# Kernel optimization log

Hardware: AMD Instinct MI355X
Metric: run time of the kernel (lower is better)

The kernel has to match this reference:

```python
import jax, jax.numpy as jnp
import numpy as np

B = 2048   # batch of sampled occupation configurations
L = 64     # nphysical (spatial orbitals / MPS sites)
P = 4      # local physical dimension (2 spin orbitals -> 4 occupations)
D = 128    # MPS bond dimension


def setup_inputs() -> dict:
    key = jax.random.key(0)
    k1, k2, k3, k4 = jax.random.split(key, 4)
    onstate = jax.random.randint(k1, (B, L), 0, P)  # occupation per site
    # flat MPS data buffer reshaped to [site, occupation, Dl, Dr];
    # scale by D**-0.5 so the length-L matrix chain stays O(1).
    site_tensors = jax.random.normal(k2, (L, P, D, D), dtype=jnp.float32) * (D ** -0.5)
    left_vec = jax.random.normal(k3, (D,), dtype=jnp.float32)
    right_vec = jax.random.normal(k4, (D,), dtype=jnp.float32)
    return {
        "onstate": onstate,
        "site_tensors": site_tensors,
        "left_vec": left_vec,
        "right_vec": right_vec,
    }


def reference(onstate, site_tensors, right_vec, left_vec=None, **_ignore):
    # keyword-robust shim not needed; real signature below
    raise NotImplementedError


def reference(onstate, site_tensors, left_vec, right_vec):
    """MPS amplitude: amp[b] = l^T (prod_i A[i, s_{b,i}]) r, evaluated as a
    left-to-right chain of gathered batched vector-matrix products."""
    batch = onstate.shape[0]
    s_seq = onstate.T.astype(jnp.int32)                      # [L, B]
    v0 = jnp.broadcast_to(left_vec, (batch, left_vec.shape[0]))  # [B, D]

    def step(v, inp):
        A_i, s_i = inp            # A_i: [P, D, D], s_i: [B]
        M = A_i[s_i]              # data-dependent gather -> [B, D, D]
        v = jnp.einsum('bd,bde->be', v, M)
        return v, None

    vL, _ = jax.lax.scan(step, v0, (site_tensors, s_seq))
    return vL @ right_vec         # [B] amplitudes
```

## Files before the change

### kernel.cpp

```cpp
#include <hip/hip_runtime.h>
#include <hip/hip_fp16.h>

constexpr int L = 64;
constexpr int P = 4;
constexpr int D = 128;
constexpr int B = 2048;
constexpr int EPW = 16;
constexpr int NG = B / EPW;

using v8h = __attribute__((ext_vector_type(8))) _Float16;
using v4h = __attribute__((ext_vector_type(4))) _Float16;
using v4f = __attribute__((ext_vector_type(4))) float;

constexpr size_t UT_OFF  = 0;
constexpr size_t WT_OFF  = 1048576;
constexpr size_t MTF_OFF = 2097152;
constexpr size_t MTB_OFF = 6291456;

constexpr int VLDS0 = 131072;
constexpr int VLDS1 = 131072 + 4096;
constexpr int PLDS  = 131072 + 8192;
constexpr int SMEM_BYTES = PLDS + L * EPW * 4;

#define WAIT_VM8   0xF78
#define WAIT_VM0   0xF70
#define WAIT_LGKM0 0xC07F

__device__ __forceinline__ void gl2lds16(const void* g, void* l) {
  __builtin_amdgcn_global_load_lds(
      (const __attribute__((address_space(1))) void*)g,
      (__attribute__((address_space(3))) void*)l, 16, 0, 0);
}

__global__ void convert_dual(const float* __restrict__ src,
                             _Float16* __restrict__ mtf,
                             _Float16* __restrict__ mtb) {
  const int mat  = blockIdx.x >> 1;
  const int half = blockIdx.x & 1;
  const int site = mat >> 2;
  const int t = threadIdx.x;
  if (site >= 32) {
    const float4* sb = (const float4*)(src + (size_t)mat * 16384);
    _Float16* bb = mtb + (size_t)(mat - 128) * 16384;
#pragma unroll
    for (int it = 0; it < 8; ++it) {
      int idx = t + (half * 8 + it) * 256;
      float4 f = sb[idx];
      v4h h4 = {(_Float16)f.x, (_Float16)f.y, (_Float16)f.z, (_Float16)f.w};
      *(v4h*)(bb + idx * 4) = h4;
    }
    return;
  }
  const float* sb = src + (size_t)mat * 16384;
  _Float16* fb = mtf + (size_t)mat * 16384;
  const int cl = t & 63;
  const int dg = t >> 6;
  const int c = half * 64 + cl;
#pragma unroll
  for (int dh = 0; dh < 4; ++dh) {
    const int d8 = dh * 4 + dg;
    v8h v;
#pragma unroll
    for (int j = 0; j < 8; ++j) v[j] = (_Float16)sb[(d8 * 8 + j) * D + c];
    *(v8h*)(fb + c * D + d8 * 8) = v;
  }
}

__global__ __launch_bounds__(512, 1) void mps_half_chain(
    const int* __restrict__ onstate, const _Float16* __restrict__ mtf,
    const _Float16* __restrict__ mtb, const float* __restrict__ left_vec,
    const float* __restrict__ right_vec, float* __restrict__ ut,
    float* __restrict__ wt) {
  extern __shared__ char smem[];
  const int tid = threadIdx.x;
  const int wave = tid >> 6, lane = tid & 63;
  const int me = lane & 15, q4 = lane >> 4;
  const bool fwd = !(blockIdx.x & 1);
  const int b0 = (blockIdx.x >> 1) * EPW;
  const _Float16* mbase = fwd ? mtf : mtb;
  const float* ivec = fwd ? left_vec : right_vec;
  float* ovec = fwd ? ut : wt;

  int* plds = (int*)(smem + PLDS);
#pragma unroll
  for (int j = 0; j < 2; ++j) {
    int idx = tid + j * 512;
    int e = idx >> 6, i = idx & 63;
    plds[i * EPW + e] = onstate[(b0 + e) * L + i];
  }
  if (tid < 256) {
    int e = tid >> 4, seg = tid & 15;
    _Float16* vp = (_Float16*)(smem + VLDS0) + e * 128 + (seg ^ (e & 7)) * 8;
#pragma unroll
    for (int j = 0; j < 8; ++j) vp[j] = (_Float16)ivec[seg * 8 + j];
  }

  char* wbuf = smem + wave * 16384;

  int soff[8];
#pragma unroll
  for (int i = 0; i < 8; ++i) {
    int u = i * 64 + lane;
    int p = u >> 7, r = u & 127, cl = r >> 3, slot = r & 7;
    soff[i] = p * 32768 + (wave * 16 + cl) * 256 + (slot ^ (cl & 7)) * 16;
  }
  auto stage = [&](int ls, int h, int z) {
    const char* gb = (const char*)mbase + (size_t)ls * 131072 + h * 128;
    char* lb = wbuf + z * 8192;
#pragma unroll
    for (int i = 0; i < 8; ++i) gl2lds16(gb + soff[i], lb + i * 1024);
  };
  auto consume = [&](int h, int z, int pm, const char* vb, v4f& acc) {
    const int s0 = h * 8 + q4, s1 = h * 8 + 4 + q4;
    v8h a0 = *(const v8h*)(vb + me * 256 + (s0 ^ (me & 7)) * 16);
    v8h a1 = *(const v8h*)(vb + me * 256 + (s1 ^ (me & 7)) * 16);
    const char* cb = wbuf + z * 8192;
#pragma unroll
    for (int p = 0; p < P; ++p) {
      const bool isp = (pm == p);
      v8h zf = {};
      v8h am0 = isp ? a0 : zf;
      v8h am1 = isp ? a1 : zf;
      const char* pb = cb + p * 2048 + me * 128;
      v8h bf0 = *(const v8h*)(pb + ((q4) ^ (me & 7)) * 16);
      v8h bf1 = *(const v8h*)(pb + ((4 + q4) ^ (me & 7)) * 16);
      acc = __builtin_amdgcn_mfma_f32_16x16x32_f16(am0, bf0, acc, 0, 0, 0);
      acc = __builtin_amdgcn_mfma_f32_16x16x32_f16(am1, bf1, acc, 0, 0, 0);
    }
  };

  __syncthreads();
  stage(fwd ? 0 : 31, 0, 0);

  const int c0 = wave * 16 + me;
  v4f accL = {0.f, 0.f, 0.f, 0.f};
  for (int site = 0; site < 32; ++site) {
    const int site_g = fwd ? site : 63 - site;
    const int ls     = fwd ? site : 31 - site;
    const int pm = plds[site_g * EPW + me];
    const char* vb = smem + ((site & 1) ? VLDS1 : VLDS0);
    v4f acc = {0.f, 0.f, 0.f, 0.f};

    stage(ls, 1, 1);
    __builtin_amdgcn_s_waitcnt(WAIT_VM8);
    __builtin_amdgcn_sched_barrier(0);
    consume(0, 0, pm, vb, acc);

    if (site < 31) {
      const int lsn = fwd ? site + 1 : 30 - site;
      __builtin_amdgcn_sched_barrier(0);
      __builtin_amdgcn_s_waitcnt(WAIT_LGKM0);
      __builtin_amdgcn_sched_barrier(0);
      stage(lsn, 0, 0);
      __builtin_amdgcn_s_waitcnt(WAIT_VM8);
      __builtin_amdgcn_sched_barrier(0);
      consume(1, 1, pm, vb, acc);
      _Float16* vn = (_Float16*)(smem + ((site & 1) ? VLDS0 : VLDS1));
#pragma unroll
      for (int r = 0; r < 4; ++r) {
        int e = q4 * 4 + r;
        vn[e * 128 + ((c0 >> 3) ^ (e & 7)) * 8 + (c0 & 7)] = (_Float16)acc[r];
      }
      __builtin_amdgcn_sched_barrier(0);
      __builtin_amdgcn_s_waitcnt(WAIT_LGKM0);
      __builtin_amdgcn_s_barrier();
      __builtin_amdgcn_sched_barrier(0);
    } else {
      __builtin_amdgcn_s_waitcnt(WAIT_VM0);
      __builtin_amdgcn_sched_barrier(0);
      consume(1, 1, pm, vb, acc);
      accL = acc;
    }
  }
#pragma unroll
  for (int r = 0; r < 4; ++r) ovec[c0 * B + b0 + q4 * 4 + r] = accL[r];
}

__global__ void combine_uw(const float* __restrict__ ut,
                           const float* __restrict__ wt,
                           float* __restrict__ out) {
  __shared__ float red[256];
  const int t = threadIdx.x;
  const int b = blockIdx.x * 64 + (t & 63);
  const int w = t >> 6;
  float s = 0.f;
#pragma unroll
  for (int i = 0; i < 32; ++i) {
    const int d = w * 32 + i;
    s += ut[d * B + b] * wt[d * B + b];
  }
  red[t] = s;
  __syncthreads();
  if (t < 64) out[b] = red[t] + red[t + 64] + red[t + 128] + red[t + 192];
}

extern "C" void kernel_launch(void* const* d_in, const int* in_sizes, int n_in,
                              void* d_out, int out_size, void* d_ws,
                              size_t ws_size, hipStream_t stream) {
  const int*   onstate      = (const int*)d_in[0];
  const float* site_tensors = (const float*)d_in[1];
  const float* left_vec     = (const float*)d_in[2];
  const float* right_vec    = (const float*)d_in[3];
  float*       out          = (float*)d_out;
  char*        ws           = (char*)d_ws;
  float*       ut           = (float*)(ws + UT_OFF);
  float*       wt           = (float*)(ws + WT_OFF);
  _Float16*    mtf          = (_Float16*)(ws + MTF_OFF);
  _Float16*    mtb          = (_Float16*)(ws + MTB_OFF);

  hipFuncSetAttribute((const void*)mps_half_chain,
                      hipFuncAttributeMaxDynamicSharedMemorySize, SMEM_BYTES);

  convert_dual<<<L * P * 2, 256, 0, stream>>>(site_tensors, mtf, mtb);
  mps_half_chain<<<2 * NG, 512, SMEM_BYTES, stream>>>(
      onstate, mtf, mtb, left_vec, right_vec, ut, wt);
  combine_uw<<<B / 64, 256, 0, stream>>>(ut, wt, out);
}
```

Before: 127.7 us.

## Stage MPS site matrices directly into registers in MFMA fragment layout

The conversion kernel now writes fp16 site matrices pre-arranged in the exact per-lane MFMA B-fragment order. The chain kernel loads each site's fragments straight into a double-buffered register bank with plain vector global loads, replacing the 128 KB LDS staging through global_load_lds. LDS use drops to a few KB, and launch bounds ask for 2 blocks per CU to raise occupancy. In exchange it holds 32 v8h registers per lane for the two banks, which raises register pressure and may cause spills. Global loads are no longer overlapped through explicit waitcnt scheduling.

```diff
diff --git a/kernel.cpp b/kernel.cpp
--- a/kernel.cpp
+++ b/kernel.cpp
@@ -9,7 +9,6 @@
 constexpr int NG = B / EPW;
 
 using v8h = __attribute__((ext_vector_type(8))) _Float16;
-using v4h = __attribute__((ext_vector_type(4))) _Float16;
 using v4f = __attribute__((ext_vector_type(4))) float;
 
 constexpr size_t UT_OFF  = 0;
@@ -17,61 +16,53 @@
 constexpr size_t MTF_OFF = 2097152;
 constexpr size_t MTB_OFF = 6291456;
 
-constexpr int VLDS0 = 131072;
-constexpr int VLDS1 = 131072 + 4096;
-constexpr int PLDS  = 131072 + 8192;
-constexpr int SMEM_BYTES = PLDS + L * EPW * 4;
-
-#define WAIT_VM8   0xF78
-#define WAIT_VM0   0xF70
 #define WAIT_LGKM0 0xC07F
-
-__device__ __forceinline__ void gl2lds16(const void* g, void* l) {
-  __builtin_amdgcn_global_load_lds(
-      (const __attribute__((address_space(1))) void*)g,
-      (__attribute__((address_space(3))) void*)l, 16, 0, 0);
-}
 
 __global__ void convert_dual(const float* __restrict__ src,
                              _Float16* __restrict__ mtf,
                              _Float16* __restrict__ mtb) {
   const int mat  = blockIdx.x >> 1;
   const int half = blockIdx.x & 1;
-  const int site = mat >> 2;
-  const int t = threadIdx.x;
+  const int site = mat >> 2, p = mat & 3;
+  const int wave = threadIdx.x >> 6, lane = threadIdx.x & 63;
+  const int me = lane & 15, q4 = lane >> 4;
+  const float* sb = src + (size_t)mat * 16384;
+
   if (site >= 32) {
-    const float4* sb = (const float4*)(src + (size_t)mat * 16384);
-    _Float16* bb = mtb + (size_t)(mat - 128) * 16384;
-#pragma unroll
-    for (int it = 0; it < 8; ++it) {
-      int idx = t + (half * 8 + it) * 256;
-      float4 f = sb[idx];
-      v4h h4 = {(_Float16)f.x, (_Float16)f.y, (_Float16)f.z, (_Float16)f.w};
-      *(v4h*)(bb + idx * 4) = h4;
+    _Float16* ob = mtb + (size_t)(site - 32) * 65536 + p * 16384;
+#pragma unroll
+    for (int i = 0; i < 4; ++i) {
+      const int kh = half * 2 + (i >> 1);
+      const int w  = (i & 1) * 4 + wave;
+      const float4* rp =
+          (const float4*)(sb + (w * 16 + me) * 128 + (kh * 4 + q4) * 8);
+      float4 f0 = rp[0], f1 = rp[1];
+      v8h v = {(_Float16)f0.x, (_Float16)f0.y, (_Float16)f0.z, (_Float16)f0.w,
+               (_Float16)f1.x, (_Float16)f1.y, (_Float16)f1.z, (_Float16)f1.w};
+      *(v8h*)(ob + kh * 4096 + w * 512 + q4 * 128 + me * 8) = v;
     }
     return;
   }
-  const float* sb = src + (size_t)mat * 16384;
-  _Float16* fb = mtf + (size_t)mat * 16384;
-  const int cl = t & 63;
-  const int dg = t >> 6;
-  const int c = half * 64 + cl;
-#pragma unroll
-  for (int dh = 0; dh < 4; ++dh) {
-    const int d8 = dh * 4 + dg;
+  _Float16* ob = mtf + (size_t)site * 65536 + p * 16384;
+#pragma unroll
+  for (int i = 0; i < 4; ++i) {
+    const int kh = half * 2 + (i >> 1);
+    const int w  = (i & 1) * 4 + wave;
     v8h v;
 #pragma unroll
-    for (int j = 0; j < 8; ++j) v[j] = (_Float16)sb[(d8 * 8 + j) * D + c];
-    *(v8h*)(fb + c * D + d8 * 8) = v;
-  }
-}
-
-__global__ __launch_bounds__(512, 1) void mps_half_chain(
+    for (int j = 0; j < 8; ++j)
+      v[j] = (_Float16)sb[((kh * 4 + q4) * 8 + j) * 128 + w * 16 + me];
+    *(v8h*)(ob + kh * 4096 + w * 512 + q4 * 128 + me * 8) = v;
+  }
+}
+
+__global__ __launch_bounds__(512, 2) void mps_half_chain(
     const int* __restrict__ onstate, const _Float16* __restrict__ mtf,
     const _Float16* __restrict__ mtb, const float* __restrict__ left_vec,
     const float* __restrict__ right_vec, float* __restrict__ ut,
     float* __restrict__ wt) {
-  extern __shared__ char smem[];
+  __shared__ _Float16 vlds[2][2048];
+  __shared__ int plds[L * EPW];
   const int tid = threadIdx.x;
   const int wave = tid >> 6, lane = tid & 63;
   const int me = lane & 15, q4 = lane >> 4;
@@ -81,7 +72,6 @@
   const float* ivec = fwd ? left_vec : right_vec;
   float* ovec = fwd ? ut : wt;
 
-  int* plds = (int*)(smem + PLDS);
 #pragma unroll
   for (int j = 0; j < 2; ++j) {
     int idx = tid + j * 512;
@@ -90,86 +80,82 @@
   }
   if (tid < 256) {
     int e = tid >> 4, seg = tid & 15;
-    _Float16* vp = (_Float16*)(smem + VLDS0) + e * 128 + (seg ^ (e & 7)) * 8;
+    _Float16* vp = &vlds[0][0] + e * 128 + (seg ^ (e & 7)) * 8;
 #pragma unroll
     for (int j = 0; j < 8; ++j) vp[j] = (_Float16)ivec[seg * 8 + j];
   }
 
-  char* wbuf = smem + wave * 16384;
-
-  int soff[8];
-#pragma unroll
-  for (int i = 0; i < 8; ++i) {
-    int u = i * 64 + lane;
-    int p = u >> 7, r = u & 127, cl = r >> 3, slot = r & 7;
-    soff[i] = p * 32768 + (wave * 16 + cl) * 256 + (slot ^ (cl & 7)) * 16;
-  }
-  auto stage = [&](int ls, int h, int z) {
-    const char* gb = (const char*)mbase + (size_t)ls * 131072 + h * 128;
-    char* lb = wbuf + z * 8192;
-#pragma unroll
-    for (int i = 0; i < 8; ++i) gl2lds16(gb + soff[i], lb + i * 1024);
+  const _Float16* gbase = mbase + wave * 512 + lane * 8;
+  auto stageR = [&](v8h (&bank)[16], int ls) {
+    const v8h* gp = (const v8h*)(gbase + (size_t)ls * 65536);
+#pragma unroll
+    for (int i = 0; i < 16; ++i) bank[i] = gp[i * 512];
   };
-  auto consume = [&](int h, int z, int pm, const char* vb, v4f& acc) {
-    const int s0 = h * 8 + q4, s1 = h * 8 + 4 + q4;
-    v8h a0 = *(const v8h*)(vb + me * 256 + (s0 ^ (me & 7)) * 16);
-    v8h a1 = *(const v8h*)(vb + me * 256 + (s1 ^ (me & 7)) * 16);
-    const char* cb = wbuf + z * 8192;
-#pragma unroll
-    for (int p = 0; p < P; ++p) {
-      const bool isp = (pm == p);
-      v8h zf = {};
-      v8h am0 = isp ? a0 : zf;
-      v8h am1 = isp ? a1 : zf;
-      const char* pb = cb + p * 2048 + me * 128;
-      v8h bf0 = *(const v8h*)(pb + ((q4) ^ (me & 7)) * 16);
-      v8h bf1 = *(const v8h*)(pb + ((4 + q4) ^ (me & 7)) * 16);
-      acc = __builtin_amdgcn_mfma_f32_16x16x32_f16(am0, bf0, acc, 0, 0, 0);
-      acc = __builtin_amdgcn_mfma_f32_16x16x32_f16(am1, bf1, acc, 0, 0, 0);
+  auto consumeSite = [&](v8h (&bank)[16], int pm, const _Float16* vb,
+                         v4f& acc) {
+#pragma unroll
+    for (int h = 0; h < 2; ++h) {
+      const int s0 = h * 8 + q4, s1 = s0 + 4;
+      v8h a0 = *(const v8h*)(vb + me * 128 + (s0 ^ (me & 7)) * 8);
+      v8h a1 = *(const v8h*)(vb + me * 128 + (s1 ^ (me & 7)) * 8);
+#pragma unroll
+      for (int p = 0; p < P; ++p) {
+        const bool isp = (pm == p);
+        v8h zf = {};
+        v8h am0 = isp ? a0 : zf;
+        v8h am1 = isp ? a1 : zf;
+        acc = __builtin_amdgcn_mfma_f32_16x16x32_f16(am0, bank[p * 4 + 2 * h],
+                                                     acc, 0, 0, 0);
+        acc = __builtin_amdgcn_mfma_f32_16x16x32_f16(
+            am1, bank[p * 4 + 2 * h + 1], acc, 0, 0, 0);
+      }
     }
   };
+  const int c0 = wave * 16 + me;
+  auto writeV = [&](_Float16* vn, const v4f& acc) {
+#pragma unroll
+    for (int r = 0; r < 4; ++r) {
+      int e = q4 * 4 + r;
+      vn[e * 128 + ((c0 >> 3) ^ (e & 7)) * 8 + (c0 & 7)] = (_Float16)acc[r];
+    }
+  };
 
   __syncthreads();
-  stage(fwd ? 0 : 31, 0, 0);
-
-  const int c0 = wave * 16 + me;
+
+  v8h bank0[16], bank1[16];
+  stageR(bank0, fwd ? 0 : 31);
+
   v4f accL = {0.f, 0.f, 0.f, 0.f};
-  for (int site = 0; site < 32; ++site) {
-    const int site_g = fwd ? site : 63 - site;
-    const int ls     = fwd ? site : 31 - site;
-    const int pm = plds[site_g * EPW + me];
-    const char* vb = smem + ((site & 1) ? VLDS1 : VLDS0);
-    v4f acc = {0.f, 0.f, 0.f, 0.f};
-
-    stage(ls, 1, 1);
-    __builtin_amdgcn_s_waitcnt(WAIT_VM8);
-    __builtin_amdgcn_sched_barrier(0);
-    consume(0, 0, pm, vb, acc);
-
-    if (site < 31) {
-      const int lsn = fwd ? site + 1 : 30 - site;
-      __builtin_amdgcn_sched_barrier(0);
-      __builtin_amdgcn_s_waitcnt(WAIT_LGKM0);
-      __builtin_amdgcn_sched_barrier(0);
-      stage(lsn, 0, 0);
-      __builtin_amdgcn_s_waitcnt(WAIT_VM8);
-      __builtin_amdgcn_sched_barrier(0);
-      consume(1, 1, pm, vb, acc);
-      _Float16* vn = (_Float16*)(smem + ((site & 1) ? VLDS0 : VLDS1));
-#pragma unroll
-      for (int r = 0; r < 4; ++r) {
-        int e = q4 * 4 + r;
-        vn[e * 128 + ((c0 >> 3) ^ (e & 7)) * 8 + (c0 & 7)] = (_Float16)acc[r];
-      }
+  for (int s2 = 0; s2 < 16; ++s2) {
+    const int se = 2 * s2, so = se + 1;
+    {
+      const int sg = fwd ? se : 63 - se;
+      const int pm = plds[sg * EPW + me];
+      stageR(bank1, fwd ? so : 31 - so);
+      v4f acc = {0.f, 0.f, 0.f, 0.f};
+      consumeSite(bank0, pm, &vlds[0][0], acc);
+      writeV(&vlds[1][0], acc);
       __builtin_amdgcn_sched_barrier(0);
       __builtin_amdgcn_s_waitcnt(WAIT_LGKM0);
       __builtin_amdgcn_s_barrier();
       __builtin_amdgcn_sched_barrier(0);
-    } else {
-      __builtin_amdgcn_s_waitcnt(WAIT_VM0);
-      __builtin_amdgcn_sched_barrier(0);
-      consume(1, 1, pm, vb, acc);
-      accL = acc;
+    }
+    {
+      const int sg = fwd ? so : 63 - so;
+      const int pm = plds[sg * EPW + me];
+      const int sn = (so + 1) & 31;
+      stageR(bank0, fwd ? sn : 31 - sn);
+      v4f acc = {0.f, 0.f, 0.f, 0.f};
+      consumeSite(bank1, pm, &vlds[1][0], acc);
+      if (so < 31) {
+        writeV(&vlds[0][0], acc);
+        __builtin_amdgcn_sched_barrier(0);
+        __builtin_amdgcn_s_waitcnt(WAIT_LGKM0);
+        __builtin_amdgcn_s_barrier();
+        __builtin_amdgcn_sched_barrier(0);
+      } else {
+        accL = acc;
+      }
     }
   }
 #pragma unroll
@@ -208,11 +194,8 @@
   _Float16*    mtf          = (_Float16*)(ws + MTF_OFF);
   _Float16*    mtb          = (_Float16*)(ws + MTB_OFF);
 
-  hipFuncSetAttribute((const void*)mps_half_chain,
-                      hipFuncAttributeMaxDynamicSharedMemorySize, SMEM_BYTES);
-
   convert_dual<<<L * P * 2, 256, 0, stream>>>(site_tensors, mtf, mtb);
-  mps_half_chain<<<2 * NG, 512, SMEM_BYTES, stream>>>(
+  mps_half_chain<<<2 * NG, 512, 0, stream>>>(
       onstate, mtf, mtb, left_vec, right_vec, ut, wt);
   combine_uw<<<B / 64, 256, 0, stream>>>(ut, wt, out);
 }
```

Result: faster. 115.9 us (-9.2%).
